# Performance work log

Measured on AMD Instinct MI355X. Metric: run time of the kernel, lower is better.

## Reference

```python
import jax, jax.numpy as jnp
import numpy as np

TAU = 0.5
EPS = 1e-8


def setup_inputs() -> dict:
    key = jax.random.key(0)
    k1, k2 = jax.random.split(key)
    N, D = 200000, 512
    z_pos = jax.random.normal(k1, (N, D), dtype=jnp.float32)
    W = jax.random.normal(k2, (D, D), dtype=jnp.float32) * (1.0 / np.sqrt(D))
    b = jnp.zeros((D,), dtype=jnp.float32)
    return {"z_pos": z_pos, "W": W, "b": b}


def reference(z_pos, W, b):
    # sample_centroid: softmax-weighted centroid (computed on detached embeddings)
    h = jax.lax.stop_gradient(z_pos)
    init_c = h.mean(axis=0)                              # [D]
    d2 = jnp.sum((h - init_c[None, :]) ** 2, axis=1)     # [N]
    w = jax.nn.softmax(-d2 / TAU)                        # [N]
    c = jnp.sum(h * w[:, None], axis=0)                  # [D]

    # SimNet: dist = 1 - cosine_similarity(proj(x), c)
    x_proj = z_pos @ W.T + b                             # [N, D]
    x_norm = jnp.maximum(jnp.linalg.norm(x_proj, axis=-1), EPS)  # [N]
    c_norm = jnp.maximum(jnp.linalg.norm(c), EPS)
    cos = (x_proj @ c) / (x_norm * c_norm)               # [N]
    dist = 1.0 - cos
    return dist
```

## Files before the change

kernel.cpp:

```cpp
#include <hip/hip_runtime.h>
#include <hip/hip_bf16.h>
#include <math.h>

#define DD 512
#define EPSF 1e-8f
#define BM 128
#define BN 128
#define BK 32
#define FBIG 3.402823466e+38f
#define NPAD 200064

typedef __bf16 bf16_t;
typedef __bf16 bf16x4 __attribute__((ext_vector_type(4)));
typedef __bf16 bf16x8 __attribute__((ext_vector_type(8)));
typedef float f32x4 __attribute__((ext_vector_type(4)));

__global__ void k_convW(const float* __restrict__ W, bf16_t* __restrict__ Wb) {
    int i = blockIdx.x * blockDim.x + threadIdx.x;
    float4 v = ((const float4*)W)[i];
    bf16x4 o;
    o[0] = (bf16_t)v.x; o[1] = (bf16_t)v.y; o[2] = (bf16_t)v.z; o[3] = (bf16_t)v.w;
    ((bf16x4*)Wb)[i] = o;
}

__global__ void k_colsum(const float* __restrict__ z, float* __restrict__ part, int N, int rpb) {
    int t = threadIdx.x;
    int b = blockIdx.x;
    int col4 = t & 127, sub = t >> 7;
    int r0 = b * rpb, r1 = min(r0 + rpb, N);
    const float4* z4 = (const float4*)z;
    float4 acc = make_float4(0.f, 0.f, 0.f, 0.f);
    #pragma unroll 4
    for (int r = r0 + sub; r < r1; r += 2) {
        float4 v = z4[(size_t)r * 128 + col4];
        acc.x += v.x; acc.y += v.y; acc.z += v.z; acc.w += v.w;
    }
    __shared__ float4 sm[128];
    if (sub == 1) sm[col4] = acc;
    __syncthreads();
    if (sub == 0) {
        float4 o = sm[col4];
        acc.x += o.x; acc.y += o.y; acc.z += o.z; acc.w += o.w;
        ((float4*)(part + (size_t)b * DD))[col4] = acc;
    }
}

__global__ void k_wcolsum(const float* __restrict__ z, const float* __restrict__ d2,
                          const float* __restrict__ d2min, const float* __restrict__ sinvp,
                          float* __restrict__ part, int N, int rpb) {
    int t = threadIdx.x;
    int b = blockIdx.x;
    int col4 = t & 127, sub = t >> 7;
    int r0 = b * rpb, r1 = min(r0 + rpb, N);
    float m  = d2min[0];
    float is = sinvp[0];
    const float4* z4 = (const float4*)z;
    float4 acc = make_float4(0.f, 0.f, 0.f, 0.f);
    #pragma unroll 4
    for (int r = r0 + sub; r < r1; r += 2) {
        float w = __expf(-2.0f * (d2[r] - m)) * is;
        float4 v = z4[(size_t)r * 128 + col4];
        acc.x += w * v.x; acc.y += w * v.y; acc.z += w * v.z; acc.w += w * v.w;
    }
    __shared__ float4 sm[128];
    if (sub == 1) sm[col4] = acc;
    __syncthreads();
    if (sub == 0) {
        float4 o = sm[col4];
        acc.x += o.x; acc.y += o.y; acc.z += o.z; acc.w += o.w;
        ((float4*)(part + (size_t)b * DD))[col4] = acc;
    }
}

__global__ void k_reduce1024(const float* __restrict__ part, float* __restrict__ outv, float scale) {
    __shared__ float sm[256];
    int j = blockIdx.x;
    int t = threadIdx.x;
    float s = part[(size_t)t * DD + j] + part[(size_t)(t + 256) * DD + j]
            + part[(size_t)(t + 512) * DD + j] + part[(size_t)(t + 768) * DD + j];
    sm[t] = s;
    __syncthreads();
    for (int st = 128; st > 0; st >>= 1) {
        if (t < st) sm[t] += sm[t + st];
        __syncthreads();
    }
    if (t == 0) outv[j] = sm[0] * scale;
}

__global__ void k_d2s(const float* __restrict__ z, const float* __restrict__ cbar,
                      float* __restrict__ d2, float* __restrict__ mpart,
                      float* __restrict__ spart, int N) {
    int t = threadIdx.x;
    int lane = t & 63, wv = t >> 6;
    int l15 = lane & 15, r4 = lane >> 4;
    const float4* c4 = (const float4*)cbar;
    float4 cf[8];
    #pragma unroll
    for (int q = 0; q < 8; ++q) cf[q] = c4[q * 16 + l15];
    int gw = (blockIdx.x * 256 + t) >> 6;
    int nw = (gridDim.x * 256) >> 6;
    float m = FBIG, s = 0.f;
    #pragma unroll 2
    for (int r = gw * 4 + r4; r < N; r += nw * 4) {
        const float4* zr = (const float4*)(z + (size_t)r * DD);
        float sum = 0.f;
        #pragma unroll
        for (int q = 0; q < 8; ++q) {
            float4 v = zr[q * 16 + l15];
            float d;
            d = v.x - cf[q].x; sum += d * d;
            d = v.y - cf[q].y; sum += d * d;
            d = v.z - cf[q].z; sum += d * d;
            d = v.w - cf[q].w; sum += d * d;
        }
        #pragma unroll
        for (int off = 1; off < 16; off <<= 1) sum += __shfl_xor(sum, off, 64);
        if (l15 == 0) d2[r] = sum;
        float nm = fminf(m, sum);
        s = s * __expf(-2.0f * (m - nm)) + __expf(-2.0f * (sum - nm));
        m = nm;
    }
    #pragma unroll
    for (int off = 16; off < 64; off <<= 1) {
        float m2 = __shfl_xor(m, off, 64);
        float s2 = __shfl_xor(s, off, 64);
        float nm = fminf(m, m2);
        s = s * __expf(-2.0f * (m - nm)) + s2 * __expf(-2.0f * (m2 - nm));
        m = nm;
    }
    __shared__ float smm[4], sms[4];
    if (lane == 0) { smm[wv] = m; sms[wv] = s; }
    __syncthreads();
    if (t == 0) {
        float M = fminf(fminf(smm[0], smm[1]), fminf(smm[2], smm[3]));
        float S = 0.f;
        #pragma unroll
        for (int i = 0; i < 4; ++i) S += sms[i] * __expf(-2.0f * (smm[i] - M));
        mpart[blockIdx.x] = M;
        spart[blockIdx.x] = S;
    }
}

__global__ void k_combine(const float* __restrict__ mpart, const float* __restrict__ spart,
                          float* __restrict__ d2min, float* __restrict__ sinvp) {
    __shared__ float smm[256], sms[256];
    int t = threadIdx.x;
    float M = FBIG, S = 0.f;
    for (int i = t; i < 1024; i += 256) {
        float m2 = mpart[i], s2 = spart[i];
        float nm = fminf(M, m2);
        S = S * __expf(-2.0f * (M - nm)) + s2 * __expf(-2.0f * (m2 - nm));
        M = nm;
    }
    smm[t] = M; sms[t] = S;
    __syncthreads();
    for (int st = 128; st > 0; st >>= 1) {
        if (t < st) {
            float m2 = smm[t + st], s2 = sms[t + st];
            float nm = fminf(smm[t], m2);
            sms[t] = sms[t] * __expf(-2.0f * (smm[t] - nm)) + s2 * __expf(-2.0f * (m2 - nm));
            smm[t] = nm;
        }
        __syncthreads();
    }
    if (t == 0) { d2min[0] = smm[0]; sinvp[0] = 1.0f / sms[0]; }
}

__global__ void k_cnorm(const float* __restrict__ cvec, float* __restrict__ outp) {
    __shared__ float sm[512];
    float v = cvec[threadIdx.x];
    sm[threadIdx.x] = v * v;
    __syncthreads();
    for (int st = 256; st > 0; st >>= 1) {
        if (threadIdx.x < st) sm[threadIdx.x] += sm[threadIdx.x + st];
        __syncthreads();
    }
    if (threadIdx.x == 0) outp[0] = 1.0f / fmaxf(sqrtf(sm[0]), EPSF);
}

__global__ __launch_bounds__(256, 3) void k_gemm(
    const float* __restrict__ z, const bf16_t* __restrict__ Wb,
    const float* __restrict__ bvec, const float* __restrict__ cvec,
    float* __restrict__ sqp, float* __restrict__ dtp, int N)
{
    __shared__ bf16_t As[BM * BK];
    __shared__ bf16_t Bs[BN * BK];
    __shared__ float psq[BM][2];
    __shared__ float pdt[BM][2];

    const int t    = threadIdx.x;
    const int lane = t & 63;
    const int wv   = t >> 6;
    const int wr   = wv >> 1;
    const int wc   = wv & 1;
    const int quad = lane >> 4;
    const int l15  = lane & 15;
    const int cb   = blockIdx.x;
    const int row0 = blockIdx.y * BM;

    const int arow = t >> 1;
    const int ah   = t & 1;
    int rowe = row0 + arow; if (rowe >= N) rowe = N - 1;
    const float4* zp4 = (const float4*)(z + (size_t)rowe * DD + ah * 16);

    const bf16_t* bp = Wb + (size_t)(cb * BN + (t >> 2)) * DD + (t & 3) * 8;

    f32x4 acc[4][4];
    #pragma unroll
    for (int a = 0; a < 4; ++a)
        #pragma unroll
        for (int b = 0; b < 4; ++b) acc[a][b] = (f32x4){0.f, 0.f, 0.f, 0.f};

    float4 v0 = zp4[0], v1 = zp4[1], v2 = zp4[2], v3 = zp4[3];

    for (int kc = 0; kc < DD; kc += BK) {
        if (kc) __syncthreads();

        #pragma unroll
        for (int q = 0; q < 2; ++q) {
            int ldsoff = __builtin_amdgcn_readfirstlane(q * 4096 + wv * 1024);
            __builtin_amdgcn_global_load_lds(
                (const __attribute__((address_space(1))) unsigned int*)(const void*)(bp + (size_t)q * 64 * DD + kc),
                (__attribute__((address_space(3))) unsigned int*)(void*)((char*)Bs + ldsoff),
                16, 0, 0);
        }
        bf16x8 lo, hi;
        lo[0]=(bf16_t)v0.x; lo[1]=(bf16_t)v0.y; lo[2]=(bf16_t)v0.z; lo[3]=(bf16_t)v0.w;
        lo[4]=(bf16_t)v1.x; lo[5]=(bf16_t)v1.y; lo[6]=(bf16_t)v1.z; lo[7]=(bf16_t)v1.w;
        hi[0]=(bf16_t)v2.x; hi[1]=(bf16_t)v2.y; hi[2]=(bf16_t)v2.z; hi[3]=(bf16_t)v2.w;
        hi[4]=(bf16_t)v3.x; hi[5]=(bf16_t)v3.y; hi[6]=(bf16_t)v3.z; hi[7]=(bf16_t)v3.w;
        *(bf16x8*)(As + arow * BK + ah * 16)     = lo;
        *(bf16x8*)(As + arow * BK + ah * 16 + 8) = hi;

        __syncthreads();

        if (kc + BK < DD) {
            int kf = (kc + BK) >> 2;
            v0 = zp4[kf]; v1 = zp4[kf + 1]; v2 = zp4[kf + 2]; v3 = zp4[kf + 3];
        }

        bf16x8 af[4];
        #pragma unroll
        for (int rt = 0; rt < 4; ++rt)
            af[rt] = *(const bf16x8*)(As + (wr * 64 + rt * 16 + l15) * BK + quad * 8);
        #pragma unroll
        for (int ct = 0; ct < 4; ++ct) {
            bf16x8 bfv = *(const bf16x8*)(Bs + (wc * 64 + ct * 16 + l15) * BK + quad * 8);
            #pragma unroll
            for (int rt = 0; rt < 4; ++rt)
                acc[rt][ct] = __builtin_amdgcn_mfma_f32_16x16x32_bf16(af[rt], bfv, acc[rt][ct], 0, 0, 0);
        }
    }

    float bc[4], cc[4];
    #pragma unroll
    for (int ct = 0; ct < 4; ++ct) {
        int col = cb * BN + wc * 64 + ct * 16 + l15;
        bc[ct] = bvec[col];
        cc[ct] = cvec[col];
    }
    #pragma unroll
    for (int rt = 0; rt < 4; ++rt) {
        #pragma unroll
        for (int rg = 0; rg < 4; ++rg) {
            float sq = 0.f, dt = 0.f;
            #pragma unroll
            for (int ct = 0; ct < 4; ++ct) {
                float x = acc[rt][ct][rg] + bc[ct];
                sq += x * x;
                dt += x * cc[ct];
            }
            #pragma unroll
            for (int off = 1; off < 16; off <<= 1) {
                sq += __shfl_xor(sq, off, 64);
                dt += __shfl_xor(dt, off, 64);
            }
            if (l15 == 0) {
                int rl = wr * 64 + rt * 16 + quad * 4 + rg;
                psq[rl][wc] = sq;
                pdt[rl][wc] = dt;
            }
        }
    }
    __syncthreads();
    if (t < BM) {
        int r = row0 + t;
        if (r < N) {
            sqp[(size_t)cb * NPAD + r] = psq[t][0] + psq[t][1];
            dtp[(size_t)cb * NPAD + r] = pdt[t][0] + pdt[t][1];
        }
    }
}

__global__ void k_final(const float* __restrict__ sqp, const float* __restrict__ dtp,
                        const float* __restrict__ cninv, float* __restrict__ out, int N) {
    int r = blockIdx.x * blockDim.x + threadIdx.x;
    if (r < N) {
        float sq = sqp[r] + sqp[NPAD + r] + sqp[2 * NPAD + r] + sqp[3 * NPAD + r];
        float dt = dtp[r] + dtp[NPAD + r] + dtp[2 * NPAD + r] + dtp[3 * NPAD + r];
        out[r] = 1.0f - dt * cninv[0] / fmaxf(sqrtf(sq), EPSF);
    }
}

extern "C" void kernel_launch(void* const* d_in, const int* in_sizes, int n_in,
                              void* d_out, int out_size, void* d_ws, size_t ws_size,
                              hipStream_t stream)
{
    const float* z = (const float*)d_in[0];
    const float* W = (const float*)d_in[1];
    const float* b = (const float*)d_in[2];
    float* out = (float*)d_out;
    int N = in_sizes[0] / DD;

    float* ws = (float*)d_ws;
    size_t off = 0;
    float* part  = ws + off; off += (size_t)1024 * DD;
    float* cbar  = ws + off; off += DD;
    float* d2    = ws + off; off += (size_t)NPAD;
    float* mpart = ws + off; off += 1024;
    float* spart = ws + off; off += 1024;
    float* d2min = ws + off; off += 1;
    float* sinvp = ws + off; off += 1;
    float* cvec  = ws + off; off += DD;
    float* cninv = ws + off; off += 1;
    off = (off + 3) & ~(size_t)3;
    float* sqp   = ws + off; off += (size_t)4 * NPAD;
    float* dtp   = ws + off; off += (size_t)4 * NPAD;
    bf16_t* Wb   = (bf16_t*)(ws + off);

    int rpb = (N + 1023) / 1024;

    k_convW<<<256, 256, 0, stream>>>(W, Wb);
    k_colsum<<<1024, 256, 0, stream>>>(z, part, N, rpb);
    k_reduce1024<<<DD, 256, 0, stream>>>(part, cbar, 1.0f / (float)N);
    k_d2s<<<1024, 256, 0, stream>>>(z, cbar, d2, mpart, spart, N);
    k_combine<<<1, 256, 0, stream>>>(mpart, spart, d2min, sinvp);
    k_wcolsum<<<1024, 256, 0, stream>>>(z, d2, d2min, sinvp, part, N, rpb);
    k_reduce1024<<<DD, 256, 0, stream>>>(part, cvec, 1.0f);
    k_cnorm<<<1, DD, 0, stream>>>(cvec, cninv);
    dim3 grid(4, (N + BM - 1) / BM);
    k_gemm<<<grid, 256, 0, stream>>>(z, Wb, b, cvec, sqp, dtp, N);
    k_final<<<(N + 255) / 256, 256, 0, stream>>>(sqp, dtp, cninv, out, N);
}
```

Measured before the change: 935.9 us.

## Materialize bf16 copy of z during column-sum pass and reuse it downstream

The first column-sum pass now also writes a bf16 copy of z into workspace. The weighted column sum and the GEMM then read this half-size copy instead of the fp32 input, and the GEMM stages its A tile with direct global-to-LDS loads like the B tile. This cuts the repeated fp32 reads of the large activation matrix, which the GEMM previously did once per column block. The cost is an extra bf16 write and a workspace-size dependency, with a fallback to the fp32 path if the workspace is too small. It also doubles the partial-block count to 2048 and raises launch bounds occupancy from 3 to 4.

```diff
diff --git a/kernel.cpp b/kernel.cpp
--- a/kernel.cpp
+++ b/kernel.cpp
@@ -8,22 +8,28 @@
 #define BN 128
 #define BK 32
 #define FBIG 3.402823466e+38f
-#define NPAD 200064
+#define NPART 2048
 
 typedef __bf16 bf16_t;
-typedef __bf16 bf16x4 __attribute__((ext_vector_type(4)));
-typedef __bf16 bf16x8 __attribute__((ext_vector_type(8)));
+typedef __bf16 bf16x4_t __attribute__((ext_vector_type(4)));
+typedef __bf16 bf16x8_t __attribute__((ext_vector_type(8)));
 typedef float f32x4 __attribute__((ext_vector_type(4)));
+
+__device__ inline float bf2f(unsigned short u) {
+    return __uint_as_float(((unsigned int)u) << 16);
+}
 
 __global__ void k_convW(const float* __restrict__ W, bf16_t* __restrict__ Wb) {
     int i = blockIdx.x * blockDim.x + threadIdx.x;
     float4 v = ((const float4*)W)[i];
-    bf16x4 o;
+    bf16x4_t o;
     o[0] = (bf16_t)v.x; o[1] = (bf16_t)v.y; o[2] = (bf16_t)v.z; o[3] = (bf16_t)v.w;
-    ((bf16x4*)Wb)[i] = o;
-}
-
-__global__ void k_colsum(const float* __restrict__ z, float* __restrict__ part, int N, int rpb) {
+    ((bf16x4_t*)Wb)[i] = o;
+}
+
+template<bool CONV>
+__global__ void k_colsum(const float* __restrict__ z, bf16_t* __restrict__ zb,
+                         float* __restrict__ part, int N, int rpb) {
     int t = threadIdx.x;
     int b = blockIdx.x;
     int col4 = t & 127, sub = t >> 7;
@@ -33,6 +39,11 @@
     #pragma unroll 4
     for (int r = r0 + sub; r < r1; r += 2) {
         float4 v = z4[(size_t)r * 128 + col4];
+        if (CONV) {
+            bf16x4_t o;
+            o[0] = (bf16_t)v.x; o[1] = (bf16_t)v.y; o[2] = (bf16_t)v.z; o[3] = (bf16_t)v.w;
+            ((bf16x4_t*)zb)[(size_t)r * 128 + col4] = o;
+        }
         acc.x += v.x; acc.y += v.y; acc.z += v.z; acc.w += v.w;
     }
     __shared__ float4 sm[128];
@@ -45,9 +56,9 @@
     }
 }
 
-__global__ void k_wcolsum(const float* __restrict__ z, const float* __restrict__ d2,
-                          const float* __restrict__ d2min, const float* __restrict__ sinvp,
-                          float* __restrict__ part, int N, int rpb) {
+__global__ void k_wcolsum_f(const float* __restrict__ z, const float* __restrict__ d2,
+                            const float* __restrict__ d2min, const float* __restrict__ sinvp,
+                            float* __restrict__ part, int N, int rpb) {
     int t = threadIdx.x;
     int b = blockIdx.x;
     int col4 = t & 127, sub = t >> 7;
@@ -72,12 +83,41 @@
     }
 }
 
-__global__ void k_reduce1024(const float* __restrict__ part, float* __restrict__ outv, float scale) {
+__global__ void k_wcolsum_b(const bf16_t* __restrict__ zb, const float* __restrict__ d2,
+                            const float* __restrict__ d2min, const float* __restrict__ sinvp,
+                            float* __restrict__ part, int N, int rpb) {
+    int t = threadIdx.x;
+    int b = blockIdx.x;
+    int col4 = t & 127, sub = t >> 7;
+    int r0 = b * rpb, r1 = min(r0 + rpb, N);
+    float m  = d2min[0];
+    float is = sinvp[0];
+    const ushort4* z4 = (const ushort4*)zb;
+    float4 acc = make_float4(0.f, 0.f, 0.f, 0.f);
+    #pragma unroll 8
+    for (int r = r0 + sub; r < r1; r += 2) {
+        float w = __expf(-2.0f * (d2[r] - m)) * is;
+        ushort4 u = z4[(size_t)r * 128 + col4];
+        acc.x += w * bf2f(u.x); acc.y += w * bf2f(u.y);
+        acc.z += w * bf2f(u.z); acc.w += w * bf2f(u.w);
+    }
+    __shared__ float4 sm[128];
+    if (sub == 1) sm[col4] = acc;
+    __syncthreads();
+    if (sub == 0) {
+        float4 o = sm[col4];
+        acc.x += o.x; acc.y += o.y; acc.z += o.z; acc.w += o.w;
+        ((float4*)(part + (size_t)b * DD))[col4] = acc;
+    }
+}
+
+__global__ void k_reduceP(const float* __restrict__ part, float* __restrict__ outv, float scale) {
     __shared__ float sm[256];
     int j = blockIdx.x;
     int t = threadIdx.x;
-    float s = part[(size_t)t * DD + j] + part[(size_t)(t + 256) * DD + j]
-            + part[(size_t)(t + 512) * DD + j] + part[(size_t)(t + 768) * DD + j];
+    float s = 0.f;
+    #pragma unroll
+    for (int p = 0; p < NPART / 256; ++p) s += part[(size_t)(p * 256 + t) * DD + j];
     sm[t] = s;
     __syncthreads();
     for (int st = 128; st > 0; st >>= 1) {
@@ -146,7 +186,7 @@
     __shared__ float smm[256], sms[256];
     int t = threadIdx.x;
     float M = FBIG, S = 0.f;
-    for (int i = t; i < 1024; i += 256) {
+    for (int i = t; i < NPART; i += 256) {
         float m2 = mpart[i], s2 = spart[i];
         float nm = fminf(M, m2);
         S = S * __expf(-2.0f * (M - nm)) + s2 * __expf(-2.0f * (m2 - nm));
@@ -178,10 +218,12 @@
     if (threadIdx.x == 0) outp[0] = 1.0f / fmaxf(sqrtf(sm[0]), EPSF);
 }
 
-__global__ __launch_bounds__(256, 3) void k_gemm(
-    const float* __restrict__ z, const bf16_t* __restrict__ Wb,
-    const float* __restrict__ bvec, const float* __restrict__ cvec,
-    float* __restrict__ sqp, float* __restrict__ dtp, int N)
+template<bool ZB>
+__global__ __launch_bounds__(256, 4) void k_gemm(
+    const float* __restrict__ z, const bf16_t* __restrict__ zb,
+    const bf16_t* __restrict__ Wb, const float* __restrict__ bvec,
+    const float* __restrict__ cvec, float* __restrict__ sqp, float* __restrict__ dtp,
+    int N, int npad)
 {
     __shared__ bf16_t As[BM * BK];
     __shared__ bf16_t Bs[BN * BK];
@@ -198,20 +240,22 @@
     const int cb   = blockIdx.x;
     const int row0 = blockIdx.y * BM;
 
+    const bf16_t* bp = Wb + (size_t)(cb * BN + (t >> 2)) * DD + (t & 3) * 8;
+    const bf16_t* ap = zb + (size_t)(row0 + (t >> 2)) * DD + (t & 3) * 8;
+
     const int arow = t >> 1;
     const int ah   = t & 1;
     int rowe = row0 + arow; if (rowe >= N) rowe = N - 1;
     const float4* zp4 = (const float4*)(z + (size_t)rowe * DD + ah * 16);
 
-    const bf16_t* bp = Wb + (size_t)(cb * BN + (t >> 2)) * DD + (t & 3) * 8;
-
     f32x4 acc[4][4];
     #pragma unroll
     for (int a = 0; a < 4; ++a)
         #pragma unroll
         for (int b = 0; b < 4; ++b) acc[a][b] = (f32x4){0.f, 0.f, 0.f, 0.f};
 
-    float4 v0 = zp4[0], v1 = zp4[1], v2 = zp4[2], v3 = zp4[3];
+    float4 v0, v1, v2, v3;
+    if (!ZB) { v0 = zp4[0]; v1 = zp4[1]; v2 = zp4[2]; v3 = zp4[3]; }
 
     for (int kc = 0; kc < DD; kc += BK) {
         if (kc) __syncthreads();
@@ -224,28 +268,39 @@
                 (__attribute__((address_space(3))) unsigned int*)(void*)((char*)Bs + ldsoff),
                 16, 0, 0);
         }
-        bf16x8 lo, hi;
-        lo[0]=(bf16_t)v0.x; lo[1]=(bf16_t)v0.y; lo[2]=(bf16_t)v0.z; lo[3]=(bf16_t)v0.w;
-        lo[4]=(bf16_t)v1.x; lo[5]=(bf16_t)v1.y; lo[6]=(bf16_t)v1.z; lo[7]=(bf16_t)v1.w;
-        hi[0]=(bf16_t)v2.x; hi[1]=(bf16_t)v2.y; hi[2]=(bf16_t)v2.z; hi[3]=(bf16_t)v2.w;
-        hi[4]=(bf16_t)v3.x; hi[5]=(bf16_t)v3.y; hi[6]=(bf16_t)v3.z; hi[7]=(bf16_t)v3.w;
-        *(bf16x8*)(As + arow * BK + ah * 16)     = lo;
-        *(bf16x8*)(As + arow * BK + ah * 16 + 8) = hi;
+        if (ZB) {
+            #pragma unroll
+            for (int q = 0; q < 2; ++q) {
+                int ldsoff = __builtin_amdgcn_readfirstlane(q * 4096 + wv * 1024);
+                __builtin_amdgcn_global_load_lds(
+                    (const __attribute__((address_space(1))) unsigned int*)(const void*)(ap + (size_t)q * 64 * DD + kc),
+                    (__attribute__((address_space(3))) unsigned int*)(void*)((char*)As + ldsoff),
+                    16, 0, 0);
+            }
+        } else {
+            bf16x8_t lo, hi;
+            lo[0]=(bf16_t)v0.x; lo[1]=(bf16_t)v0.y; lo[2]=(bf16_t)v0.z; lo[3]=(bf16_t)v0.w;
+            lo[4]=(bf16_t)v1.x; lo[5]=(bf16_t)v1.y; lo[6]=(bf16_t)v1.z; lo[7]=(bf16_t)v1.w;
+            hi[0]=(bf16_t)v2.x; hi[1]=(bf16_t)v2.y; hi[2]=(bf16_t)v2.z; hi[3]=(bf16_t)v2.w;
+            hi[4]=(bf16_t)v3.x; hi[5]=(bf16_t)v3.y; hi[6]=(bf16_t)v3.z; hi[7]=(bf16_t)v3.w;
+            *(bf16x8_t*)(As + arow * BK + ah * 16)     = lo;
+            *(bf16x8_t*)(As + arow * BK + ah * 16 + 8) = hi;
+        }
 
         __syncthreads();
 
-        if (kc + BK < DD) {
+        if (!ZB && kc + BK < DD) {
             int kf = (kc + BK) >> 2;
             v0 = zp4[kf]; v1 = zp4[kf + 1]; v2 = zp4[kf + 2]; v3 = zp4[kf + 3];
         }
 
-        bf16x8 af[4];
+        bf16x8_t af[4];
         #pragma unroll
         for (int rt = 0; rt < 4; ++rt)
-            af[rt] = *(const bf16x8*)(As + (wr * 64 + rt * 16 + l15) * BK + quad * 8);
+            af[rt] = *(const bf16x8_t*)(As + (wr * 64 + rt * 16 + l15) * BK + quad * 8);
         #pragma unroll
         for (int ct = 0; ct < 4; ++ct) {
-            bf16x8 bfv = *(const bf16x8*)(Bs + (wc * 64 + ct * 16 + l15) * BK + quad * 8);
+            bf16x8_t bfv = *(const bf16x8_t*)(Bs + (wc * 64 + ct * 16 + l15) * BK + quad * 8);
             #pragma unroll
             for (int rt = 0; rt < 4; ++rt)
                 acc[rt][ct] = __builtin_amdgcn_mfma_f32_16x16x32_bf16(af[rt], bfv, acc[rt][ct], 0, 0, 0);
@@ -286,18 +341,19 @@
     if (t < BM) {
         int r = row0 + t;
         if (r < N) {
-            sqp[(size_t)cb * NPAD + r] = psq[t][0] + psq[t][1];
-            dtp[(size_t)cb * NPAD + r] = pdt[t][0] + pdt[t][1];
+            sqp[(size_t)cb * npad + r] = psq[t][0] + psq[t][1];
+            dtp[(size_t)cb * npad + r] = pdt[t][0] + pdt[t][1];
         }
     }
 }
 
 __global__ void k_final(const float* __restrict__ sqp, const float* __restrict__ dtp,
-                        const float* __restrict__ cninv, float* __restrict__ out, int N) {
+                        const float* __restrict__ cninv, float* __restrict__ out,
+                        int N, int npad) {
     int r = blockIdx.x * blockDim.x + threadIdx.x;
     if (r < N) {
-        float sq = sqp[r] + sqp[NPAD + r] + sqp[2 * NPAD + r] + sqp[3 * NPAD + r];
-        float dt = dtp[r] + dtp[NPAD + r] + dtp[2 * NPAD + r] + dtp[3 * NPAD + r];
+        float sq = sqp[r] + sqp[(size_t)npad + r] + sqp[2 * (size_t)npad + r] + sqp[3 * (size_t)npad + r];
+        float dt = dtp[r] + dtp[(size_t)npad + r] + dtp[2 * (size_t)npad + r] + dtp[3 * (size_t)npad + r];
         out[r] = 1.0f - dt * cninv[0] / fmaxf(sqrtf(sq), EPSF);
     }
 }
@@ -311,34 +367,41 @@
     const float* b = (const float*)d_in[2];
     float* out = (float*)d_out;
     int N = in_sizes[0] / DD;
+    int npad = ((N + BM - 1) / BM) * BM;
 
     float* ws = (float*)d_ws;
     size_t off = 0;
-    float* part  = ws + off; off += (size_t)1024 * DD;
+    float* part  = ws + off; off += (size_t)NPART * DD;
     float* cbar  = ws + off; off += DD;
-    float* d2    = ws + off; off += (size_t)NPAD;
-    float* mpart = ws + off; off += 1024;
-    float* spart = ws + off; off += 1024;
+    float* d2    = ws + off; off += (size_t)npad;
+    float* mpart = ws + off; off += NPART;
+    float* spart = ws + off; off += NPART;
     float* d2min = ws + off; off += 1;
     float* sinvp = ws + off; off += 1;
     float* cvec  = ws + off; off += DD;
     float* cninv = ws + off; off += 1;
     off = (off + 3) & ~(size_t)3;
-    float* sqp   = ws + off; off += (size_t)4 * NPAD;
-    float* dtp   = ws + off; off += (size_t)4 * NPAD;
-    bf16_t* Wb   = (bf16_t*)(ws + off);
-
-    int rpb = (N + 1023) / 1024;
+    float* sqp   = ws + off; off += (size_t)4 * npad;
+    float* dtp   = ws + off; off += (size_t)4 * npad;
+    bf16_t* Wb   = (bf16_t*)(ws + off); off += (size_t)DD * DD / 2;
+    bf16_t* zb   = (bf16_t*)(ws + off);
+    size_t need_bytes = (off + (size_t)npad * DD / 2) * sizeof(float);
+    const bool use_zb = ws_size >= need_bytes;
+
+    int rpb = (N + NPART - 1) / NPART;
 
     k_convW<<<256, 256, 0, stream>>>(W, Wb);
-    k_colsum<<<1024, 256, 0, stream>>>(z, part, N, rpb);
-    k_reduce1024<<<DD, 256, 0, stream>>>(part, cbar, 1.0f / (float)N);
-    k_d2s<<<1024, 256, 0, stream>>>(z, cbar, d2, mpart, spart, N);
+    if (use_zb) k_colsum<true ><<<NPART, 256, 0, stream>>>(z, zb, part, N, rpb);
+    else        k_colsum<false><<<NPART, 256, 0, stream>>>(z, zb, part, N, rpb);
+    k_reduceP<<<DD, 256, 0, stream>>>(part, cbar, 1.0f / (float)N);
+    k_d2s<<<NPART, 256, 0, stream>>>(z, cbar, d2, mpart, spart, N);
     k_combine<<<1, 256, 0, stream>>>(mpart, spart, d2min, sinvp);
-    k_wcolsum<<<1024, 256, 0, stream>>>(z, d2, d2min, sinvp, part, N, rpb);
-    k_reduce1024<<<DD, 256, 0, stream>>>(part, cvec, 1.0f);
+    if (use_zb) k_wcolsum_b<<<NPART, 256, 0, stream>>>(zb, d2, d2min, sinvp, part, N, rpb);
+    else        k_wcolsum_f<<<NPART, 256, 0, stream>>>(z,  d2, d2min, sinvp, part, N, rpb);
+    k_reduceP<<<DD, 256, 0, stream>>>(part, cvec, 1.0f);
     k_cnorm<<<1, DD, 0, stream>>>(cvec, cninv);
-    dim3 grid(4, (N + BM - 1) / BM);
-    k_gemm<<<grid, 256, 0, stream>>>(z, Wb, b, cvec, sqp, dtp, N);
-    k_final<<<(N + 255) / 256, 256, 0, stream>>>(sqp, dtp, cninv, out, N);
-}
+    dim3 grid(4, npad / BM);
+    if (use_zb) k_gemm<true ><<<grid, 256, 0, stream>>>(z, zb, Wb, b, cvec, sqp, dtp, N, npad);
+    else        k_gemm<false><<<grid, 256, 0, stream>>>(z, zb, Wb, b, cvec, sqp, dtp, N, npad);
+    k_final<<<(N + 255) / 256, 256, 0, stream>>>(sqp, dtp, cninv, out, N, npad);
+}
```

Measured after the change: 903.3 us. 1.04x faster.
